# Kernel optimization log

Measured on AMD Instinct MI355X. Metric: run time of the kernel, lower is better.

Reference implementation:

```python
import jax, jax.numpy as jnp
import numpy as np

N = 100000   # nodes
E = 1600000  # edges (avg degree 16)
F_IN = 64
H = 64
C = 40       # classes


def setup_inputs() -> dict:
    key = jax.random.key(0)
    ks = jax.random.split(key, 12)

    def lin(k, out_d, in_d):
        kw, kb = jax.random.split(k)
        W = jax.random.normal(kw, (out_d, in_d), jnp.float32) / jnp.sqrt(jnp.float32(in_d))
        b = jnp.zeros((out_d,), jnp.float32)
        return W, b

    Wl1, b1 = lin(ks[2], H, F_IN)
    Wr1, _ = lin(ks[3], H, F_IN)
    Wl2, b2 = lin(ks[4], H, H)
    Wr2, _ = lin(ks[5], H, H)
    Wl3, b3 = lin(ks[6], C, H)
    Wr3, _ = lin(ks[7], C, H)

    return {
        "x": jax.random.normal(ks[0], (N, F_IN), jnp.float32),
        "edge_index": jax.random.randint(ks[1], (2, E), 0, N, jnp.int32),
        "Wl1": Wl1, "Wr1": Wr1, "b1": b1,
        "Wl2": Wl2, "Wr2": Wr2, "b2": b2,
        "Wl3": Wl3, "Wr3": Wr3, "b3": b3,
    }


def _sage_conv(x, src, dst, Wl, Wr, b, n_nodes):
    # PyG SAGEConv (aggr='mean'): out = lin_l(mean_{j in N(i)} x_j) + lin_r(x_i)
    msg = x[src]                                                   # [E, F] gather
    agg_sum = jax.ops.segment_sum(msg, dst, num_segments=n_nodes)  # [N, F]
    deg = jax.ops.segment_sum(jnp.ones((src.shape[0],), x.dtype), dst,
                              num_segments=n_nodes)                # [N]
    agg = agg_sum / jnp.maximum(deg, 1.0)[:, None]                 # mean aggregation
    return agg @ Wl.T + b + x @ Wr.T


def reference(x, edge_index, Wl1, Wr1, b1, Wl2, Wr2, b2, Wl3, Wr3, b3):
    src, dst = edge_index[0], edge_index[1]
    n = x.shape[0]
    # dropout is identity in eval mode (training=self.training)
    h = jax.nn.relu(_sage_conv(x, src, dst, Wl1, Wr1, b1, n))
    h = jax.nn.relu(_sage_conv(h, src, dst, Wl2, Wr2, b2, n))
    h = _sage_conv(h, src, dst, Wl3, Wr3, b3, n)
    return jax.nn.log_softmax(h, axis=1)
```

## Files before the change

### kernel.cpp

```cpp
#include <hip/hip_runtime.h>
#include <hip/hip_bf16.h>
#include <math.h>


#define BK_SHIFT 7
#define BK_NODES 128
#define NB_MAX   1024
#define BBLK     256

typedef __attribute__((ext_vector_type(8))) short short8;
typedef __attribute__((ext_vector_type(4))) float f32x4;

__device__ inline float blo(unsigned v) { union { unsigned u; float f; } c; c.u = v << 16; return c.f; }
__device__ inline float bhi(unsigned v) { union { unsigned u; float f; } c; c.u = v & 0xFFFF0000u; return c.f; }
__device__ inline unsigned short f2bf(float f) {
    union { float f; unsigned u; } c; c.f = f;
    unsigned r = (c.u + 0x7FFFu + ((c.u >> 16) & 1u)) >> 16;
    return (unsigned short)r;
}

__global__ __launch_bounds__(256) void prep_kernel(const int* __restrict__ dstA, int* __restrict__ cnts,
                                                   int E, int NB,
                                                   const float* __restrict__ x, unsigned short* __restrict__ Xb, int n8,
                                                   const float* __restrict__ Wl1, const float* __restrict__ Wr1,
                                                   const float* __restrict__ Wl2, const float* __restrict__ Wr2,
                                                   const float* __restrict__ Wl3, const float* __restrict__ Wr3,
                                                   unsigned short* __restrict__ Wb1,
                                                   unsigned short* __restrict__ Wb2,
                                                   unsigned short* __restrict__ Wb3) {
    int b = blockIdx.x, t = threadIdx.x;
    if (b < BBLK) {
        __shared__ int lc[NB_MAX];
        for (int i = t; i < NB_MAX; i += 256) lc[i] = 0;
        __syncthreads();
        int chunk = (E + BBLK - 1) / BBLK;
        int e0 = b * chunk, e1 = min(E, e0 + chunk);
        for (int e = e0 + t; e < e1; e += 256)
            atomicAdd(&lc[dstA[e] >> BK_SHIFT], 1);
        __syncthreads();
        for (int i = t; i < NB_MAX; i += 256) cnts[b * NB_MAX + i] = lc[i];
    } else if (b < BBLK + 88) {
        int i = (b - BBLK) * 256 + t;
        if (i < 8192) {
            int c = i >> 7, k = i & 127;
            float v = (k < 64) ? Wl1[c * 64 + k] : Wr1[c * 64 + k - 64];
            Wb1[i] = f2bf(v);
        } else if (i < 16384) {
            int j = i - 8192;
            int c = j >> 7, k = j & 127;
            float v = (k < 64) ? Wl2[c * 64 + k] : Wr2[c * 64 + k - 64];
            Wb2[j] = f2bf(v);
        } else if (i < 22528) {
            int j = i - 16384;
            int c = j >> 6, k = j & 63;
            float v = 0.f;
            if (c < 40) v = Wl3[c * 64 + k];
            else if (c >= 48 && c < 88) v = Wr3[(c - 48) * 64 + k];
            Wb3[j] = f2bf(v);
        }
    } else {
        for (int i = (b - (BBLK + 88)) * 256 + t; i < n8; i += 1024 * 256) {
            const float* p = x + (size_t)i * 8;
            float4 a = *(const float4*)p;
            float4 bq = *(const float4*)(p + 4);
            uint4 o;
            o.x = f2bf(a.x) | ((unsigned)f2bf(a.y) << 16);
            o.y = f2bf(a.z) | ((unsigned)f2bf(a.w) << 16);
            o.z = f2bf(bq.x) | ((unsigned)f2bf(bq.y) << 16);
            o.w = f2bf(bq.z) | ((unsigned)f2bf(bq.w) << 16);
            *(uint4*)(Xb + (size_t)i * 8) = o;
        }
    }
}

__global__ __launch_bounds__(256) void colscan_kernel(const int* __restrict__ cnts,
                                                      int* __restrict__ lpre,
                                                      int* __restrict__ bcount) {
    __shared__ int s[BBLK];
    int j = blockIdx.x, t = threadIdx.x;
    int v = cnts[t * NB_MAX + j];
    s[t] = v;
    __syncthreads();
    for (int off = 1; off < BBLK; off <<= 1) {
        int x = 0;
        if (t >= off) x = s[t - off];
        __syncthreads();
        s[t] += x;
        __syncthreads();
    }
    lpre[t * NB_MAX + j] = s[t] - v;
    if (t == BBLK - 1) bcount[j] = s[t];
}

__global__ __launch_bounds__(1024) void bscan_kernel(const int* __restrict__ bcount,
                                                     int* __restrict__ bbase, int NB, int E) {
    __shared__ int s[1024];
    int t = threadIdx.x;
    int v = (t < NB) ? bcount[t] : 0;
    s[t] = v;
    __syncthreads();
    for (int off = 1; off < 1024; off <<= 1) {
        int x = 0;
        if (t >= off) x = s[t - off];
        __syncthreads();
        s[t] += x;
        __syncthreads();
    }
    if (t < NB) bbase[t] = s[t] - v;
    if (t == 0) bbase[NB] = E;
}

__global__ __launch_bounds__(512) void bin_kernel(const int* __restrict__ srcA,
                                                  const int* __restrict__ dstA,
                                                  const int* __restrict__ lpre,
                                                  const int* __restrict__ bbase,
                                                  int* __restrict__ binned, int E, int NB) {
    __shared__ int lc[NB_MAX];
    int b = blockIdx.x, t = threadIdx.x;
    for (int i = t; i < NB; i += 512)
        lc[i] = lpre[b * NB_MAX + i] + bbase[i];
    __syncthreads();
    int chunk = (E + BBLK - 1) / BBLK;
    int e0 = b * chunk, e1 = min(E, e0 + chunk);
    for (int e = e0 + t; e < e1; e += 512) {
        int d = dstA[e];
        int bk = d >> BK_SHIFT;
        int pos = atomicAdd(&lc[bk], 1);
        binned[pos] = srcA[e] | ((d & (BK_NODES - 1)) << 24);
    }
}

__global__ __launch_bounds__(256) void bsort_kernel(const int* __restrict__ binned,
                                                    const int* __restrict__ bbase,
                                                    int* __restrict__ col,
                                                    int* __restrict__ row_start, int N) {
    __shared__ int cnt[1024];
    __shared__ int keybase[1024];
    __shared__ int ts[256];
    int b = blockIdx.x, t = threadIdx.x;
    int e0 = bbase[b], e1 = bbase[b + 1];
    for (int i = t; i < 1024; i += 256) cnt[i] = 0;
    __syncthreads();
    for (int e = e0 + t; e < e1; e += 256) {
        unsigned p = (unsigned)binned[e];
        int key = (int)((p >> 24) << 3) | (int)(((p & 0xFFFFFFu) >> 14) & 7u);
        atomicAdd(&cnt[key], 1);
    }
    __syncthreads();
    int c0 = cnt[4 * t], c1 = cnt[4 * t + 1], c2 = cnt[4 * t + 2], c3 = cnt[4 * t + 3];
    int sum = c0 + c1 + c2 + c3;
    ts[t] = sum;
    __syncthreads();
    for (int off = 1; off < 256; off <<= 1) {
        int x = 0;
        if (t >= off) x = ts[t - off];
        __syncthreads();
        ts[t] += x;
        __syncthreads();
    }
    int run = e0 + ts[t] - sum;
    keybase[4 * t] = run;     run += c0;
    keybase[4 * t + 1] = run; run += c1;
    keybase[4 * t + 2] = run; run += c2;
    keybase[4 * t + 3] = run;
    __syncthreads();
    if (t < BK_NODES) {
        int node = b * BK_NODES + t;
        if (node < N) row_start[node] = keybase[t * 8];
    }
    if (b == gridDim.x - 1 && t == 0) row_start[N] = e1;
    for (int i = t; i < 1024; i += 256) cnt[i] = 0;
    __syncthreads();
    for (int e = e0 + t; e < e1; e += 256) {
        unsigned p = (unsigned)binned[e];
        int key = (int)((p >> 24) << 3) | (int)(((p & 0xFFFFFFu) >> 14) & 7u);
        int pos = keybase[key] + atomicAdd(&cnt[key], 1);
        col[pos] = p & 0xFFFFFF;
    }
}

__global__ __launch_bounds__(256) void agg64_kernel(const unsigned short* __restrict__ X,
                                                    const int* __restrict__ rs,
                                                    const int* __restrict__ col,
                                                    unsigned short* __restrict__ OUT, int n) {
    int t = threadIdx.x;
    int node = blockIdx.x * 32 + (t >> 3);
    if (node >= n) return;
    int lane = t & 7;
    int s = rs[node], d = rs[node + 1] - s;
    const unsigned short* lp = X + lane * 8;
    float a0 = 0.f, a1 = 0.f, a2 = 0.f, a3 = 0.f, a4 = 0.f, a5 = 0.f, a6 = 0.f, a7 = 0.f;
    int j = 0;
    for (; j + 3 < d; j += 4) {
        int c0 = col[s + j], c1 = col[s + j + 1];
        int c2 = col[s + j + 2], c3 = col[s + j + 3];
        uint4 q0 = *(const uint4*)(lp + (size_t)c0 * 64);
        uint4 q1 = *(const uint4*)(lp + (size_t)c1 * 64);
        uint4 q2 = *(const uint4*)(lp + (size_t)c2 * 64);
        uint4 q3 = *(const uint4*)(lp + (size_t)c3 * 64);
        a0 += (blo(q0.x) + blo(q1.x)) + (blo(q2.x) + blo(q3.x));
        a1 += (bhi(q0.x) + bhi(q1.x)) + (bhi(q2.x) + bhi(q3.x));
        a2 += (blo(q0.y) + blo(q1.y)) + (blo(q2.y) + blo(q3.y));
        a3 += (bhi(q0.y) + bhi(q1.y)) + (bhi(q2.y) + bhi(q3.y));
        a4 += (blo(q0.z) + blo(q1.z)) + (blo(q2.z) + blo(q3.z));
        a5 += (bhi(q0.z) + bhi(q1.z)) + (bhi(q2.z) + bhi(q3.z));
        a6 += (blo(q0.w) + blo(q1.w)) + (blo(q2.w) + blo(q3.w));
        a7 += (bhi(q0.w) + bhi(q1.w)) + (bhi(q2.w) + bhi(q3.w));
    }
    for (; j < d; ++j) {
        int c0 = col[s + j];
        uint4 q0 = *(const uint4*)(lp + (size_t)c0 * 64);
        a0 += blo(q0.x); a1 += bhi(q0.x); a2 += blo(q0.y); a3 += bhi(q0.y);
        a4 += blo(q0.z); a5 += bhi(q0.z); a6 += blo(q0.w); a7 += bhi(q0.w);
    }
    float w = 1.f / (float)(d > 0 ? d : 1);
    a0 *= w; a1 *= w; a2 *= w; a3 *= w; a4 *= w; a5 *= w; a6 *= w; a7 *= w;
    uint4 o;
    o.x = f2bf(a0) | ((unsigned)f2bf(a1) << 16);
    o.y = f2bf(a2) | ((unsigned)f2bf(a3) << 16);
    o.z = f2bf(a4) | ((unsigned)f2bf(a5) << 16);
    o.w = f2bf(a6) | ((unsigned)f2bf(a7) << 16);
    *(uint4*)(OUT + (size_t)node * 64 + lane * 8) = o;
}

__global__ __launch_bounds__(256) void linmfma12_kernel(const unsigned short* __restrict__ A,
                                                        const unsigned short* __restrict__ X,
                                                        const unsigned short* __restrict__ Wb,
                                                        const float* __restrict__ bias,
                                                        unsigned short* __restrict__ OUT,
                                                        int N) {
    __shared__ unsigned short Ys[64][136];
    __shared__ unsigned short Ws[64][136];
    int t = threadIdx.x;
    int rowbase = blockIdx.x * 64;
#pragma unroll
    for (int it = 0; it < 4; ++it) {
        int idx = it * 256 + t;
        int row = idx >> 4, c = idx & 15;
        int grow = rowbase + row;
        if (grow >= N) grow = N - 1;
        const unsigned short* src = (c < 8) ? (A + (size_t)grow * 64 + c * 8)
                                            : (X + (size_t)grow * 64 + (c - 8) * 8);
        *(short8*)&Ys[row][c * 8] = *(const short8*)src;
        *(short8*)&Ws[row][c * 8] = *(const short8*)(Wb + (size_t)row * 128 + c * 8);
    }
    __syncthreads();
    int l = t & 63, w = t >> 6;
    int lrow = l & 15, lk = l >> 4;
    f32x4 acc0 = {0.f, 0.f, 0.f, 0.f};
    f32x4 acc1 = acc0, acc2 = acc0, acc3 = acc0;
#pragma unroll
    for (int kk = 0; kk < 4; ++kk) {
        int ko = kk * 32 + lk * 8;
        short8 a  = *(const short8*)&Ys[16 * w + lrow][ko];
        short8 b0 = *(const short8*)&Ws[lrow][ko];
        short8 b1 = *(const short8*)&Ws[16 + lrow][ko];
        short8 b2 = *(const short8*)&Ws[32 + lrow][ko];
        short8 b3 = *(const short8*)&Ws[48 + lrow][ko];
        acc0 = __builtin_amdgcn_mfma_f32_16x16x32_bf16(a, b0, acc0, 0, 0, 0);
        acc1 = __builtin_amdgcn_mfma_f32_16x16x32_bf16(a, b1, acc1, 0, 0, 0);
        acc2 = __builtin_amdgcn_mfma_f32_16x16x32_bf16(a, b2, acc2, 0, 0, 0);
        acc3 = __builtin_amdgcn_mfma_f32_16x16x32_bf16(a, b3, acc3, 0, 0, 0);
    }
#define EPI12(nt, accv)                                                   \
    {                                                                     \
        int colc = 16 * (nt) + lrow;                                      \
        float bv = bias[colc];                                            \
        _Pragma("unroll") for (int i = 0; i < 4; ++i) {                   \
            int grow = rowbase + 16 * w + lk * 4 + i;                     \
            if (grow < N) {                                               \
                float v = fmaxf(accv[i] + bv, 0.f);                       \
                OUT[(size_t)grow * 64 + colc] = f2bf(v);                  \
            }                                                             \
        }                                                                 \
    }
    EPI12(0, acc0) EPI12(1, acc1) EPI12(2, acc2) EPI12(3, acc3)
#undef EPI12
}

__global__ __launch_bounds__(256) void linmfma3_kernel(const unsigned short* __restrict__ H,
                                                       const unsigned short* __restrict__ Wb3,
                                                       const float* __restrict__ b3,
                                                       unsigned short* __restrict__ Z,
                                                       float* __restrict__ R,
                                                       int N) {
    __shared__ unsigned short Ys[64][72];
    __shared__ unsigned short Ws[96][72];
    int t = threadIdx.x;
    int rowbase = blockIdx.x * 64;
#pragma unroll
    for (int it = 0; it < 2; ++it) {
        int idx = it * 256 + t;
        int row = idx >> 3, c = idx & 7;
        int grow = rowbase + row;
        if (grow >= N) grow = N - 1;
        *(short8*)&Ys[row][c * 8] = *(const short8*)(H + (size_t)grow * 64 + c * 8);
    }
#pragma unroll
    for (int it = 0; it < 3; ++it) {
        int idx = it * 256 + t;
        int row = idx >> 3, c = idx & 7;
        *(short8*)&Ws[row][c * 8] = *(const short8*)(Wb3 + (size_t)row * 64 + c * 8);
    }
    __syncthreads();
    int l = t & 63, w = t >> 6;
    int lrow = l & 15, lk = l >> 4;
    f32x4 acc0 = {0.f, 0.f, 0.f, 0.f};
    f32x4 acc1 = acc0, acc2 = acc0, acc3 = acc0, acc4 = acc0, acc5 = acc0;
#pragma unroll
    for (int kk = 0; kk < 2; ++kk) {
        int ko = kk * 32 + lk * 8;
        short8 a  = *(const short8*)&Ys[16 * w + lrow][ko];
        short8 b0 = *(const short8*)&Ws[lrow][ko];
        short8 b1 = *(const short8*)&Ws[16 + lrow][ko];
        short8 b2 = *(const short8*)&Ws[32 + lrow][ko];
        short8 b3f = *(const short8*)&Ws[48 + lrow][ko];
        short8 b4 = *(const short8*)&Ws[64 + lrow][ko];
        short8 b5 = *(const short8*)&Ws[80 + lrow][ko];
        acc0 = __builtin_amdgcn_mfma_f32_16x16x32_bf16(a, b0, acc0, 0, 0, 0);
        acc1 = __builtin_amdgcn_mfma_f32_16x16x32_bf16(a, b1, acc1, 0, 0, 0);
        acc2 = __builtin_amdgcn_mfma_f32_16x16x32_bf16(a, b2, acc2, 0, 0, 0);
        acc3 = __builtin_amdgcn_mfma_f32_16x16x32_bf16(a, b3f, acc3, 0, 0, 0);
        acc4 = __builtin_amdgcn_mfma_f32_16x16x32_bf16(a, b4, acc4, 0, 0, 0);
        acc5 = __builtin_amdgcn_mfma_f32_16x16x32_bf16(a, b5, acc5, 0, 0, 0);
    }
#define EPI3(nt, accv)                                                     \
    {                                                                      \
        int colc = 16 * (nt) + lrow;                                       \
        _Pragma("unroll") for (int i = 0; i < 4; ++i) {                    \
            int grow = rowbase + 16 * w + lk * 4 + i;                      \
            if (grow < N) {                                                \
                float v = accv[i];                                         \
                if (colc < 40) {                                           \
                    Z[(size_t)grow * 40 + colc] = f2bf(v);                 \
                } else if (colc >= 48 && colc < 88) {                      \
                    R[(size_t)grow * 40 + (colc - 48)] = v + b3[colc - 48];\
                }                                                          \
            }                                                              \
        }                                                                  \
    }
    EPI3(0, acc0) EPI3(1, acc1) EPI3(2, acc2) EPI3(3, acc3) EPI3(4, acc4) EPI3(5, acc5)
#undef EPI3
}

__global__ __launch_bounds__(256) void agg40lsm_kernel(const unsigned short* __restrict__ Z,
                                                       const int* __restrict__ rs,
                                                       const int* __restrict__ col,
                                                       float* __restrict__ out, int n) {
    int t = threadIdx.x;
    int node = blockIdx.x * 32 + (t >> 3);
    if (node >= n) return;
    int lane = t & 7;
    bool act = lane < 5;
    int s = rs[node], d = rs[node + 1] - s;
    const unsigned short* lp = Z + lane * 8;
    float a0 = 0.f, a1 = 0.f, a2 = 0.f, a3 = 0.f, a4 = 0.f, a5 = 0.f, a6 = 0.f, a7 = 0.f;
    int j = 0;
    for (; j + 3 < d; j += 4) {
        int c0 = col[s + j], c1 = col[s + j + 1];
        int c2 = col[s + j + 2], c3 = col[s + j + 3];
        if (act) {
            uint4 q0 = *(const uint4*)(lp + (size_t)c0 * 40);
            uint4 q1 = *(const uint4*)(lp + (size_t)c1 * 40);
            uint4 q2 = *(const uint4*)(lp + (size_t)c2 * 40);
            uint4 q3 = *(const uint4*)(lp + (size_t)c3 * 40);
            a0 += (blo(q0.x) + blo(q1.x)) + (blo(q2.x) + blo(q3.x));
            a1 += (bhi(q0.x) + bhi(q1.x)) + (bhi(q2.x) + bhi(q3.x));
            a2 += (blo(q0.y) + blo(q1.y)) + (blo(q2.y) + blo(q3.y));
            a3 += (bhi(q0.y) + bhi(q1.y)) + (bhi(q2.y) + bhi(q3.y));
            a4 += (blo(q0.z) + blo(q1.z)) + (blo(q2.z) + blo(q3.z));
            a5 += (bhi(q0.z) + bhi(q1.z)) + (bhi(q2.z) + bhi(q3.z));
            a6 += (blo(q0.w) + blo(q1.w)) + (blo(q2.w) + blo(q3.w));
            a7 += (bhi(q0.w) + bhi(q1.w)) + (bhi(q2.w) + bhi(q3.w));
        }
    }
    for (; j < d; ++j) {
        int c0 = col[s + j];
        if (act) {
            uint4 q0 = *(const uint4*)(lp + (size_t)c0 * 40);
            a0 += blo(q0.x); a1 += bhi(q0.x); a2 += blo(q0.y); a3 += bhi(q0.y);
            a4 += blo(q0.z); a5 += bhi(q0.z); a6 += blo(q0.w); a7 += bhi(q0.w);
        }
    }
    float w = 1.f / (float)(d > 0 ? d : 1);
    if (act) {
        float* op = out + (size_t)node * 40 + lane * 8;
        float4 r0 = *(const float4*)op;
        float4 r1 = *(const float4*)(op + 4);
        a0 = a0 * w + r0.x; a1 = a1 * w + r0.y; a2 = a2 * w + r0.z; a3 = a3 * w + r0.w;
        a4 = a4 * w + r1.x; a5 = a5 * w + r1.y; a6 = a6 * w + r1.z; a7 = a7 * w + r1.w;
    }
    float mx = act ? fmaxf(fmaxf(fmaxf(a0, a1), fmaxf(a2, a3)),
                           fmaxf(fmaxf(a4, a5), fmaxf(a6, a7))) : -3.4e38f;
#pragma unroll
    for (int off = 1; off < 8; off <<= 1) mx = fmaxf(mx, __shfl_xor(mx, off, 8));
    float ssum = act ? (expf(a0 - mx) + expf(a1 - mx) + expf(a2 - mx) + expf(a3 - mx) +
                        expf(a4 - mx) + expf(a5 - mx) + expf(a6 - mx) + expf(a7 - mx)) : 0.f;
#pragma unroll
    for (int off = 1; off < 8; off <<= 1) ssum += __shfl_xor(ssum, off, 8);
    float lg = mx + logf(ssum);
    if (act) {
        float* op = out + (size_t)node * 40 + lane * 8;
        float4 o0, o1;
        o0.x = a0 - lg; o0.y = a1 - lg; o0.z = a2 - lg; o0.w = a3 - lg;
        o1.x = a4 - lg; o1.y = a5 - lg; o1.z = a6 - lg; o1.w = a7 - lg;
        *(float4*)op = o0;
        *(float4*)(op + 4) = o1;
    }
}

extern "C" void kernel_launch(void* const* d_in, const int* in_sizes, int n_in,
                              void* d_out, int out_size, void* d_ws, size_t ws_size,
                              hipStream_t stream) {
    const float* x   = (const float*)d_in[0];
    const int*   ei  = (const int*)d_in[1];
    const float* Wl1 = (const float*)d_in[2];
    const float* Wr1 = (const float*)d_in[3];
    const float* b1  = (const float*)d_in[4];
    const float* Wl2 = (const float*)d_in[5];
    const float* Wr2 = (const float*)d_in[6];
    const float* b2  = (const float*)d_in[7];
    const float* Wl3 = (const float*)d_in[8];
    const float* Wr3 = (const float*)d_in[9];
    const float* b3  = (const float*)d_in[10];
    float* out = (float*)d_out;

    const int N = in_sizes[0] / 64;
    const int E = in_sizes[1] / 2;
    const int NB = (N + BK_NODES - 1) / BK_NODES;
    const int* srcA = ei;
    const int* dstA = ei + E;

    char* ws = (char*)d_ws;
    size_t off = 0;
    auto alloc = [&](size_t bytes) {
        off = (off + 255) & ~(size_t)255;
        char* p = ws + off;
        off += bytes;
        return p;
    };
    int* cnts      = (int*)alloc((size_t)BBLK * NB_MAX * 4);
    int* lpre      = (int*)alloc((size_t)BBLK * NB_MAX * 4);
    int* bcount    = (int*)alloc((size_t)(NB_MAX + 1) * 4);
    int* bbase     = (int*)alloc((size_t)(NB_MAX + 1) * 4);
    int* binned    = (int*)alloc((size_t)E * 4);
    int* col       = (int*)alloc((size_t)E * 4);
    int* row_start = (int*)alloc((size_t)(N + 1) * 4);
    unsigned short* Xb  = (unsigned short*)alloc((size_t)N * 64 * 2);
    unsigned short* AGG = (unsigned short*)alloc((size_t)N * 64 * 2);
    unsigned short* Hb  = (unsigned short*)alloc((size_t)N * 64 * 2);
    unsigned short* Zb  = (unsigned short*)alloc((size_t)N * 40 * 2);
    unsigned short* Wb1 = (unsigned short*)alloc(8192 * 2);
    unsigned short* Wb2 = (unsigned short*)alloc(8192 * 2);
    unsigned short* Wb3 = (unsigned short*)alloc(6144 * 2);

    prep_kernel<<<BBLK + 88 + 1024, 256, 0, stream>>>(dstA, cnts, E, NB, x, Xb, N * 64 / 8,
                                                      Wl1, Wr1, Wl2, Wr2, Wl3, Wr3, Wb1, Wb2, Wb3);
    colscan_kernel<<<NB, BBLK, 0, stream>>>(cnts, lpre, bcount);
    bscan_kernel<<<1, 1024, 0, stream>>>(bcount, bbase, NB, E);
    bin_kernel<<<BBLK, 512, 0, stream>>>(srcA, dstA, lpre, bbase, binned, E, NB);
    bsort_kernel<<<NB, 256, 0, stream>>>(binned, bbase, col, row_start, N);

    int gridA = (N + 31) / 32;
    int gridM = (N + 63) / 64;

    agg64_kernel<<<gridA, 256, 0, stream>>>(Xb, row_start, col, AGG, N);
    linmfma12_kernel<<<gridM, 256, 0, stream>>>(AGG, Xb, Wb1, b1, Hb, N);

    agg64_kernel<<<gridA, 256, 0, stream>>>(Hb, row_start, col, AGG, N);
    linmfma12_kernel<<<gridM, 256, 0, stream>>>(AGG, Hb, Wb2, b2, Hb, N);

    linmfma3_kernel<<<gridM, 256, 0, stream>>>(Hb, Wb3, b3, Zb, out, N);
    agg40lsm_kernel<<<gridA, 256, 0, stream>>>(Zb, row_start, col, out, N);
}
```

Measured before the change: 261.6 us.

## Fuse layer-2 and layer-3 linear transforms into one kernel via LDS

Replaces the separate layer-2 linear kernel and the layer-3 projection kernel with a single kernel. The ReLU'd layer-2 output for each 64-row tile is written back into shared memory and fed straight into the layer-3 MFMA GEMM. This removes one kernel launch and the global write and re-read of the hidden activations. In exchange, shared memory per block grows to roughly 48 KB, which may lower occupancy. Correctness relies on each wave reading back only the rows it wrote itself, since there is no block barrier between the two GEMMs.

```diff
diff --git a/kernel.cpp b/kernel.cpp
--- a/kernel.cpp
+++ b/kernel.cpp
@@ -278,51 +278,84 @@
 #undef EPI12
 }
 
-__global__ __launch_bounds__(256) void linmfma3_kernel(const unsigned short* __restrict__ H,
-                                                       const unsigned short* __restrict__ Wb3,
-                                                       const float* __restrict__ b3,
-                                                       unsigned short* __restrict__ Z,
-                                                       float* __restrict__ R,
-                                                       int N) {
-    __shared__ unsigned short Ys[64][72];
-    __shared__ unsigned short Ws[96][72];
+__global__ __launch_bounds__(256) void lin23_kernel(const unsigned short* __restrict__ A,
+                                                    const unsigned short* __restrict__ X,
+                                                    const unsigned short* __restrict__ Wb2,
+                                                    const float* __restrict__ bias2,
+                                                    const unsigned short* __restrict__ Wb3,
+                                                    const float* __restrict__ b3,
+                                                    unsigned short* __restrict__ Z,
+                                                    float* __restrict__ R,
+                                                    int N) {
+    __shared__ unsigned short Ys[64][136];
+    __shared__ unsigned short Ws[64][136];
+    __shared__ unsigned short W3[96][72];
     int t = threadIdx.x;
     int rowbase = blockIdx.x * 64;
 #pragma unroll
-    for (int it = 0; it < 2; ++it) {
+    for (int it = 0; it < 4; ++it) {
         int idx = it * 256 + t;
-        int row = idx >> 3, c = idx & 7;
+        int row = idx >> 4, c = idx & 15;
         int grow = rowbase + row;
         if (grow >= N) grow = N - 1;
-        *(short8*)&Ys[row][c * 8] = *(const short8*)(H + (size_t)grow * 64 + c * 8);
+        const unsigned short* src = (c < 8) ? (A + (size_t)grow * 64 + c * 8)
+                                            : (X + (size_t)grow * 64 + (c - 8) * 8);
+        *(short8*)&Ys[row][c * 8] = *(const short8*)src;
+        *(short8*)&Ws[row][c * 8] = *(const short8*)(Wb2 + (size_t)row * 128 + c * 8);
     }
 #pragma unroll
     for (int it = 0; it < 3; ++it) {
         int idx = it * 256 + t;
         int row = idx >> 3, c = idx & 7;
-        *(short8*)&Ws[row][c * 8] = *(const short8*)(Wb3 + (size_t)row * 64 + c * 8);
+        *(short8*)&W3[row][c * 8] = *(const short8*)(Wb3 + (size_t)row * 64 + c * 8);
     }
     __syncthreads();
     int l = t & 63, w = t >> 6;
     int lrow = l & 15, lk = l >> 4;
     f32x4 acc0 = {0.f, 0.f, 0.f, 0.f};
-    f32x4 acc1 = acc0, acc2 = acc0, acc3 = acc0, acc4 = acc0, acc5 = acc0;
-#pragma unroll
-    for (int kk = 0; kk < 2; ++kk) {
+    f32x4 acc1 = acc0, acc2 = acc0, acc3 = acc0;
+#pragma unroll
+    for (int kk = 0; kk < 4; ++kk) {
         int ko = kk * 32 + lk * 8;
         short8 a  = *(const short8*)&Ys[16 * w + lrow][ko];
         short8 b0 = *(const short8*)&Ws[lrow][ko];
         short8 b1 = *(const short8*)&Ws[16 + lrow][ko];
         short8 b2 = *(const short8*)&Ws[32 + lrow][ko];
-        short8 b3f = *(const short8*)&Ws[48 + lrow][ko];
-        short8 b4 = *(const short8*)&Ws[64 + lrow][ko];
-        short8 b5 = *(const short8*)&Ws[80 + lrow][ko];
+        short8 b3v = *(const short8*)&Ws[48 + lrow][ko];
         acc0 = __builtin_amdgcn_mfma_f32_16x16x32_bf16(a, b0, acc0, 0, 0, 0);
         acc1 = __builtin_amdgcn_mfma_f32_16x16x32_bf16(a, b1, acc1, 0, 0, 0);
         acc2 = __builtin_amdgcn_mfma_f32_16x16x32_bf16(a, b2, acc2, 0, 0, 0);
-        acc3 = __builtin_amdgcn_mfma_f32_16x16x32_bf16(a, b3f, acc3, 0, 0, 0);
-        acc4 = __builtin_amdgcn_mfma_f32_16x16x32_bf16(a, b4, acc4, 0, 0, 0);
-        acc5 = __builtin_amdgcn_mfma_f32_16x16x32_bf16(a, b5, acc5, 0, 0, 0);
+        acc3 = __builtin_amdgcn_mfma_f32_16x16x32_bf16(a, b3v, acc3, 0, 0, 0);
+    }
+#define EPIH(nt, accv)                                                    \
+    {                                                                     \
+        int colc = 16 * (nt) + lrow;                                      \
+        float bv = bias2[colc];                                           \
+        _Pragma("unroll") for (int i = 0; i < 4; ++i) {                   \
+            int row = 16 * w + lk * 4 + i;                                \
+            Ys[row][colc] = f2bf(fmaxf(accv[i] + bv, 0.f));               \
+        }                                                                 \
+    }
+    EPIH(0, acc0) EPIH(1, acc1) EPIH(2, acc2) EPIH(3, acc3)
+#undef EPIH
+    f32x4 z0 = {0.f, 0.f, 0.f, 0.f};
+    f32x4 z1 = z0, z2 = z0, z3 = z0, z4 = z0, z5 = z0;
+#pragma unroll
+    for (int kk = 0; kk < 2; ++kk) {
+        int ko = kk * 32 + lk * 8;
+        short8 a  = *(const short8*)&Ys[16 * w + lrow][ko];
+        short8 b0 = *(const short8*)&W3[lrow][ko];
+        short8 b1 = *(const short8*)&W3[16 + lrow][ko];
+        short8 b2 = *(const short8*)&W3[32 + lrow][ko];
+        short8 b3v = *(const short8*)&W3[48 + lrow][ko];
+        short8 b4 = *(const short8*)&W3[64 + lrow][ko];
+        short8 b5 = *(const short8*)&W3[80 + lrow][ko];
+        z0 = __builtin_amdgcn_mfma_f32_16x16x32_bf16(a, b0, z0, 0, 0, 0);
+        z1 = __builtin_amdgcn_mfma_f32_16x16x32_bf16(a, b1, z1, 0, 0, 0);
+        z2 = __builtin_amdgcn_mfma_f32_16x16x32_bf16(a, b2, z2, 0, 0, 0);
+        z3 = __builtin_amdgcn_mfma_f32_16x16x32_bf16(a, b3v, z3, 0, 0, 0);
+        z4 = __builtin_amdgcn_mfma_f32_16x16x32_bf16(a, b4, z4, 0, 0, 0);
+        z5 = __builtin_amdgcn_mfma_f32_16x16x32_bf16(a, b5, z5, 0, 0, 0);
     }
 #define EPI3(nt, accv)                                                     \
     {                                                                      \
@@ -339,7 +372,7 @@
             }                                                              \
         }                                                                  \
     }
-    EPI3(0, acc0) EPI3(1, acc1) EPI3(2, acc2) EPI3(3, acc3) EPI3(4, acc4) EPI3(5, acc5)
+    EPI3(0, z0) EPI3(1, z1) EPI3(2, z2) EPI3(3, z3) EPI3(4, z4) EPI3(5, z5)
 #undef EPI3
 }
 
@@ -468,8 +501,7 @@
     linmfma12_kernel<<<gridM, 256, 0, stream>>>(AGG, Xb, Wb1, b1, Hb, N);
 
     agg64_kernel<<<gridA, 256, 0, stream>>>(Hb, row_start, col, AGG, N);
-    linmfma12_kernel<<<gridM, 256, 0, stream>>>(AGG, Hb, Wb2, b2, Hb, N);
-
-    linmfma3_kernel<<<gridM, 256, 0, stream>>>(Hb, Wb3, b3, Zb, out, N);
+    lin23_kernel<<<gridM, 256, 0, stream>>>(AGG, Hb, Wb2, b2, Wb3, b3, Zb, out, N);
+
     agg40lsm_kernel<<<gridA, 256, 0, stream>>>(Zb, row_start, col, out, N);
 }
```

New measurement: 259.8 us. About the same (-0.7%).
